# Performance work log

Measured on AMD Instinct MI355X. Metric: run time of the kernel, lower is better.

Reference implementation:

```python
import jax, jax.numpy as jnp
import numpy as np

IN_FEATURES = 4096
OUT_FEATURES = 4096
MAX_RANK = 32
ALPHA = 32
SCALING = ALPHA / MAX_RANK  # 1.0


def setup_inputs() -> dict:
    key = jax.random.key(0)
    k_x, k_u, k_v = jax.random.split(key, 3)
    x = jax.random.normal(k_x, (4, 2048, IN_FEATURES), dtype=jnp.float32)
    U = jax.random.normal(k_u, (OUT_FEATURES, MAX_RANK), dtype=jnp.float32) * 0.01
    S = jnp.ones((MAX_RANK,), dtype=jnp.float32)
    V = jax.random.normal(k_v, (MAX_RANK, IN_FEATURES), dtype=jnp.float32) * 0.01
    return {"x": x, "U": U, "S": S, "V": V}


def reference(x, U, S, V):
    # Original: W = U @ diag(S) @ V ; out = (x @ W.T) * scaling  (dropout=0 -> Identity)
    # Mathematically identical factored form: ((x @ V^T) * S) @ U^T * scaling.
    h = jnp.einsum('bsi,ri->bsr', x, V)        # [B,S,rank]
    h = h * S                                   # scale by singular values
    out = jnp.einsum('bsr,or->bso', h, U)       # [B,S,out]
    return out * SCALING
```

## Files before the change

kernel.cpp:

```cpp
#include <hip/hip_runtime.h>
#include <hip/hip_bf16.h>

typedef __bf16 bf16x8 __attribute__((ext_vector_type(8)));
typedef float  f32x4  __attribute__((ext_vector_type(4)));

#define IN_F   4096
#define OUT_F  4096
#define RANK   32

__device__ __forceinline__ bf16x8 cvt8(float4 a, float4 b) {
    bf16x8 r;
    r[0] = (__bf16)a.x; r[1] = (__bf16)a.y; r[2] = (__bf16)a.z; r[3] = (__bf16)a.w;
    r[4] = (__bf16)b.x; r[5] = (__bf16)b.y; r[6] = (__bf16)b.z; r[7] = (__bf16)b.w;
    return r;
}

__device__ __forceinline__ void gl_lds16(const float* g, void* l) {
    __builtin_amdgcn_global_load_lds(
        (const __attribute__((address_space(1))) char*)g,
        (__attribute__((address_space(3))) char*)l, 16, 0, 0);
}

template <int KS>
__global__ __launch_bounds__(256, 2)
void lora_h(const float* __restrict__ X, const float* __restrict__ S,
            const float* __restrict__ V, float* __restrict__ Hpart)
{
    constexpr int F    = IN_F / KS;
    constexpr int NCHK = F / 64;

    __shared__ float4 XB[3][4][2][2][64];
    __shared__ float4 VB[3][2][2][2][64];

    const int tid  = threadIdx.x;
    const int wave = tid >> 6;
    const int lane = tid & 63;
    const int r    = lane & 15;
    const int kg   = lane >> 4;

    const int t0    = blockIdx.x * 64;
    const int fbase = blockIdx.y * F;

    const float s_lo = S[r];
    const float s_hi = S[16 + r];

    auto stage = [&](int c, int nb) {
        const int fc = fbase + ((c + blockIdx.x) & (NCHK - 1)) * 64;
        #pragma unroll
        for (int t = 0; t < 6; ++t) {
            const int inst = wave * 6 + t;
            if (inst < 16) {
                const int tt = inst >> 2, s = (inst >> 1) & 1, h2 = inst & 1;
                gl_lds16(X + (size_t)(t0 + tt * 16 + r) * IN_F
                           + fc + s * 32 + h2 * 16 + kg * 4,
                         (void*)&XB[nb][tt][s][h2][0]);
            } else {
                const int v = inst - 16;
                const int vr = v >> 2, s = (v >> 1) & 1, h2 = v & 1;
                gl_lds16(V + (size_t)(vr * 16 + r) * IN_F
                           + fc + s * 32 + h2 * 16 + kg * 4,
                         (void*)&VB[nb][vr][s][h2][0]);
            }
        }
    };

    const int h  = kg >> 1;
    const int qb = (kg & 1) * 2;

    f32x4 acc[2] = {};

    auto compute = [&](int cur) {
        #pragma unroll
        for (int s = 0; s < 2; ++s) {
            float4 x0 = *(const float4*)&XB[cur][wave][s][h][qb * 16 + r];
            float4 x1 = *(const float4*)&XB[cur][wave][s][h][(qb + 1) * 16 + r];
            bf16x8 xb = cvt8(x0, x1);
            #pragma unroll
            for (int rh = 0; rh < 2; ++rh) {
                float4 v0 = *(const float4*)&VB[cur][rh][s][h][qb * 16 + r];
                float4 v1 = *(const float4*)&VB[cur][rh][s][h][(qb + 1) * 16 + r];
                acc[rh] = __builtin_amdgcn_mfma_f32_16x16x32_bf16(
                              xb, cvt8(v0, v1), acc[rh], 0, 0, 0);
            }
        }
    };

    stage(0, 0);
    stage(1, 1);

    for (int c = 0; c < NCHK; ++c) {
        if (c + 2 < NCHK) {
            stage(c + 2, (c + 2) % 3);
            asm volatile("s_waitcnt vmcnt(12)" ::: "memory");
        } else if (c + 1 < NCHK) {
            asm volatile("s_waitcnt vmcnt(6)" ::: "memory");
        } else {
            asm volatile("s_waitcnt vmcnt(0)" ::: "memory");
        }
        __builtin_amdgcn_s_barrier();
        __builtin_amdgcn_sched_barrier(0);
        compute(c % 3);
        __builtin_amdgcn_s_barrier();
    }

    float* Hq = Hpart + ((size_t)blockIdx.y * 8192 + t0) * RANK;
    #pragma unroll
    for (int j = 0; j < 4; ++j) {
        const int tok = wave * 16 + kg * 4 + j;
        Hq[(size_t)tok * RANK + r]      = acc[0][j] * s_lo;
        Hq[(size_t)tok * RANK + 16 + r] = acc[1][j] * s_hi;
    }
}

template <int NKS>
__global__ __launch_bounds__(256)
void lora_hred(const float* __restrict__ Hpart, float* __restrict__ H)
{
    const int idx = blockIdx.x * 256 + threadIdx.x;
    const float4* hp = reinterpret_cast<const float4*>(Hpart);
    float4 v = hp[idx];
    #pragma unroll
    for (int k = 1; k < NKS; ++k) {
        float4 p = hp[(size_t)k * 65536 + idx];
        v.x += p.x; v.y += p.y; v.z += p.z; v.w += p.w;
    }
    reinterpret_cast<float4*>(H)[idx] = v;
}

__global__ __launch_bounds__(256, 4)
void lora_out(const float* __restrict__ H, const float* __restrict__ U,
              float* __restrict__ Out)
{
    __shared__ float Hs[128][33];

    const int tid  = threadIdx.x;
    const int wave = tid >> 6;
    const int lane = tid & 63;
    const int r    = lane & 15;
    const int kg   = lane >> 4;

    const int tt = blockIdx.x >> 6;
    const int cq = blockIdx.x & 63;
    const int t0 = tt * 128;
    const int c0 = cq * 64;

    float4 ua[4][2];
    #pragma unroll
    for (int b = 0; b < 4; ++b) {
        const float4* up = reinterpret_cast<const float4*>(
            U + (size_t)(c0 + b * 16 + r) * RANK + kg * 8);
        ua[b][0] = up[0];
        ua[b][1] = up[1];
    }

    const float4* hsrc = reinterpret_cast<const float4*>(H + (size_t)t0 * RANK);
    #pragma unroll
    for (int k4 = 0; k4 < 4; ++k4) {
        const int fidx = tid + k4 * 256;
        float4 v = hsrc[fidx];
        const int tok = fidx >> 3;
        const int rr  = (fidx & 7) * 4;
        Hs[tok][rr] = v.x; Hs[tok][rr + 1] = v.y;
        Hs[tok][rr + 2] = v.z; Hs[tok][rr + 3] = v.w;
    }
    __syncthreads();

    bf16x8 ub[4];
    #pragma unroll
    for (int b = 0; b < 4; ++b) ub[b] = cvt8(ua[b][0], ua[b][1]);

    #pragma unroll
    for (int ai = 0; ai < 2; ++ai) {
        const int a = wave + ai * 4;
        bf16x8 hb;
        #pragma unroll
        for (int j = 0; j < 8; ++j) hb[j] = (__bf16)Hs[a * 16 + r][kg * 8 + j];
        float* orow = Out + (size_t)(t0 + a * 16 + r) * OUT_F + c0 + kg * 4;
        #pragma unroll
        for (int b = 0; b < 4; ++b) {
            f32x4 d = {0.f, 0.f, 0.f, 0.f};
            d = __builtin_amdgcn_mfma_f32_16x16x32_bf16(ub[b], hb, d, 0, 0, 0);
            *reinterpret_cast<float4*>(orow + b * 16) = *reinterpret_cast<float4*>(&d);
        }
    }
}

extern "C" void kernel_launch(void* const* d_in, const int* in_sizes, int n_in,
                              void* d_out, int out_size, void* d_ws, size_t ws_size,
                              hipStream_t stream) {
    const float* X = (const float*)d_in[0];
    const float* U = (const float*)d_in[1];
    const float* S = (const float*)d_in[2];
    const float* V = (const float*)d_in[3];
    float* Out = (float*)d_out;

    float* H     = (float*)d_ws;
    float* Hpart = (float*)d_ws + 262144;

    if (ws_size >= (size_t)5 * 1024 * 1024) {
        lora_h<4><<<dim3(128, 4), 256, 0, stream>>>(X, S, V, Hpart);
        lora_hred<4><<<256, 256, 0, stream>>>(Hpart, H);
        lora_out<<<4096, 256, 0, stream>>>(H, U, Out);
    } else {
        lora_h<1><<<dim3(128, 1), 256, 0, stream>>>(X, S, V, H);
        lora_out<<<4096, 256, 0, stream>>>(H, U, Out);
    }
}
```

Measured before the change: 68.32 us.

## Retile LoRA kernels: V in registers, 32-token blocks, wider output tiles

```diff
diff --git a/kernel.cpp b/kernel.cpp
--- a/kernel.cpp
+++ b/kernel.cpp
@@ -27,10 +27,9 @@
             const float* __restrict__ V, float* __restrict__ Hpart)
 {
     constexpr int F    = IN_F / KS;
-    constexpr int NCHK = F / 64;
-
-    __shared__ float4 XB[3][4][2][2][64];
-    __shared__ float4 VB[3][2][2][2][64];
+    constexpr int NCHK = F / 256;
+
+    __shared__ float4 XB[2][2][8][2][64];
 
     const int tid  = threadIdx.x;
     const int wave = tid >> 6;
@@ -38,78 +37,71 @@
     const int r    = lane & 15;
     const int kg   = lane >> 4;
 
-    const int t0    = blockIdx.x * 64;
+    const int tt = wave & 1;
+    const int rh = wave >> 1;
+
+    const int t0    = blockIdx.x * 32;
     const int fbase = blockIdx.y * F;
 
-    const float s_lo = S[r];
-    const float s_hi = S[16 + r];
-
     auto stage = [&](int c, int nb) {
-        const int fc = fbase + ((c + blockIdx.x) & (NCHK - 1)) * 64;
-        #pragma unroll
-        for (int t = 0; t < 6; ++t) {
-            const int inst = wave * 6 + t;
-            if (inst < 16) {
-                const int tt = inst >> 2, s = (inst >> 1) & 1, h2 = inst & 1;
-                gl_lds16(X + (size_t)(t0 + tt * 16 + r) * IN_F
-                           + fc + s * 32 + h2 * 16 + kg * 4,
-                         (void*)&XB[nb][tt][s][h2][0]);
-            } else {
-                const int v = inst - 16;
-                const int vr = v >> 2, s = (v >> 1) & 1, h2 = v & 1;
-                gl_lds16(V + (size_t)(vr * 16 + r) * IN_F
-                           + fc + s * 32 + h2 * 16 + kg * 4,
-                         (void*)&VB[nb][vr][s][h2][0]);
-            }
+        const int fc = fbase + ((c + blockIdx.x) & (NCHK - 1)) * 256;
+        #pragma unroll
+        for (int t = 0; t < 8; ++t) {
+            const int inst = wave * 8 + t;
+            const int ti = inst >> 4, s = (inst >> 1) & 7, h2 = inst & 1;
+            gl_lds16(X + (size_t)(t0 + ti * 16 + r) * IN_F
+                       + fc + s * 32 + h2 * 16 + kg * 4,
+                     (void*)&XB[nb][ti][s][h2][0]);
+        }
+    };
+
+    float4 vv[16];
+    auto vload = [&](int c) {
+        const int fc = fbase + ((c + blockIdx.x) & (NCHK - 1)) * 256;
+        const float* vrow = V + (size_t)(rh * 16 + r) * IN_F + fc + kg * 8;
+        #pragma unroll
+        for (int s = 0; s < 8; ++s) {
+            const float4* vp = reinterpret_cast<const float4*>(vrow + s * 32);
+            vv[2 * s]     = vp[0];
+            vv[2 * s + 1] = vp[1];
         }
     };
 
     const int h  = kg >> 1;
     const int qb = (kg & 1) * 2;
 
-    f32x4 acc[2] = {};
+    f32x4 acc = {0.f, 0.f, 0.f, 0.f};
 
     auto compute = [&](int cur) {
         #pragma unroll
-        for (int s = 0; s < 2; ++s) {
-            float4 x0 = *(const float4*)&XB[cur][wave][s][h][qb * 16 + r];
-            float4 x1 = *(const float4*)&XB[cur][wave][s][h][(qb + 1) * 16 + r];
-            bf16x8 xb = cvt8(x0, x1);
-            #pragma unroll
-            for (int rh = 0; rh < 2; ++rh) {
-                float4 v0 = *(const float4*)&VB[cur][rh][s][h][qb * 16 + r];
-                float4 v1 = *(const float4*)&VB[cur][rh][s][h][(qb + 1) * 16 + r];
-                acc[rh] = __builtin_amdgcn_mfma_f32_16x16x32_bf16(
-                              xb, cvt8(v0, v1), acc[rh], 0, 0, 0);
-            }
+        for (int s = 0; s < 8; ++s) {
+            float4 x0 = *(const float4*)&XB[cur][tt][s][h][qb * 16 + r];
+            float4 x1 = *(const float4*)&XB[cur][tt][s][h][(qb + 1) * 16 + r];
+            acc = __builtin_amdgcn_mfma_f32_16x16x32_bf16(
+                      cvt8(x0, x1), cvt8(vv[2 * s], vv[2 * s + 1]), acc, 0, 0, 0);
         }
     };
 
     stage(0, 0);
-    stage(1, 1);
-
     for (int c = 0; c < NCHK; ++c) {
-        if (c + 2 < NCHK) {
-            stage(c + 2, (c + 2) % 3);
-            asm volatile("s_waitcnt vmcnt(12)" ::: "memory");
-        } else if (c + 1 < NCHK) {
-            asm volatile("s_waitcnt vmcnt(6)" ::: "memory");
+        vload(c);
+        if (c + 1 < NCHK) {
+            stage(c + 1, (c + 1) & 1);
+            asm volatile("s_waitcnt vmcnt(8)" ::: "memory");
         } else {
             asm volatile("s_waitcnt vmcnt(0)" ::: "memory");
         }
         __builtin_amdgcn_s_barrier();
         __builtin_amdgcn_sched_barrier(0);
-        compute(c % 3);
+        compute(c & 1);
         __builtin_amdgcn_s_barrier();
     }
 
-    float* Hq = Hpart + ((size_t)blockIdx.y * 8192 + t0) * RANK;
-    #pragma unroll
-    for (int j = 0; j < 4; ++j) {
-        const int tok = wave * 16 + kg * 4 + j;
-        Hq[(size_t)tok * RANK + r]      = acc[0][j] * s_lo;
-        Hq[(size_t)tok * RANK + 16 + r] = acc[1][j] * s_hi;
-    }
+    const float sr = S[rh * 16 + r];
+    float* Hq = Hpart + ((size_t)blockIdx.y * 8192 + t0 + tt * 16) * RANK;
+    #pragma unroll
+    for (int j = 0; j < 4; ++j)
+        Hq[(size_t)(kg * 4 + j) * RANK + rh * 16 + r] = acc[j] * sr;
 }
 
 template <int NKS>
@@ -131,7 +123,7 @@
 void lora_out(const float* __restrict__ H, const float* __restrict__ U,
               float* __restrict__ Out)
 {
-    __shared__ float Hs[128][33];
+    __shared__ float Hs[32][33];
 
     const int tid  = threadIdx.x;
     const int wave = tid >> 6;
@@ -139,48 +131,49 @@
     const int r    = lane & 15;
     const int kg   = lane >> 4;
 
-    const int tt = blockIdx.x >> 6;
-    const int cq = blockIdx.x & 63;
-    const int t0 = tt * 128;
-    const int c0 = cq * 64;
-
-    float4 ua[4][2];
-    #pragma unroll
-    for (int b = 0; b < 4; ++b) {
-        const float4* up = reinterpret_cast<const float4*>(
-            U + (size_t)(c0 + b * 16 + r) * RANK + kg * 8);
-        ua[b][0] = up[0];
-        ua[b][1] = up[1];
-    }
-
-    const float4* hsrc = reinterpret_cast<const float4*>(H + (size_t)t0 * RANK);
-    #pragma unroll
-    for (int k4 = 0; k4 < 4; ++k4) {
-        const int fidx = tid + k4 * 256;
-        float4 v = hsrc[fidx];
-        const int tok = fidx >> 3;
-        const int rr  = (fidx & 7) * 4;
+    const int tt = blockIdx.x >> 2;
+    const int cq = blockIdx.x & 3;
+    const int t0 = tt * 32;
+
+    {
+        float4 v = reinterpret_cast<const float4*>(H + (size_t)t0 * RANK)[tid];
+        const int tok = tid >> 3;
+        const int rr  = (tid & 7) * 4;
         Hs[tok][rr] = v.x; Hs[tok][rr + 1] = v.y;
         Hs[tok][rr + 2] = v.z; Hs[tok][rr + 3] = v.w;
     }
     __syncthreads();
 
-    bf16x8 ub[4];
-    #pragma unroll
-    for (int b = 0; b < 4; ++b) ub[b] = cvt8(ua[b][0], ua[b][1]);
-
-    #pragma unroll
-    for (int ai = 0; ai < 2; ++ai) {
-        const int a = wave + ai * 4;
-        bf16x8 hb;
-        #pragma unroll
-        for (int j = 0; j < 8; ++j) hb[j] = (__bf16)Hs[a * 16 + r][kg * 8 + j];
-        float* orow = Out + (size_t)(t0 + a * 16 + r) * OUT_F + c0 + kg * 4;
+    bf16x8 hb[2];
+    #pragma unroll
+    for (int a = 0; a < 2; ++a)
+        #pragma unroll
+        for (int j = 0; j < 8; ++j) hb[a][j] = (__bf16)Hs[a * 16 + r][kg * 8 + j];
+
+    const int wc0 = cq * 1024 + wave * 256;
+
+    #pragma unroll
+    for (int g = 0; g < 4; ++g) {
+        float4 u0[4], u1[4];
         #pragma unroll
         for (int b = 0; b < 4; ++b) {
-            f32x4 d = {0.f, 0.f, 0.f, 0.f};
-            d = __builtin_amdgcn_mfma_f32_16x16x32_bf16(ub[b], hb, d, 0, 0, 0);
-            *reinterpret_cast<float4*>(orow + b * 16) = *reinterpret_cast<float4*>(&d);
+            const float4* up = reinterpret_cast<const float4*>(
+                U + (size_t)(wc0 + g * 64 + b * 16 + r) * RANK + kg * 8);
+            u0[b] = up[0];
+            u1[b] = up[1];
+        }
+        #pragma unroll
+        for (int b = 0; b < 4; ++b) {
+            bf16x8 ub = cvt8(u0[b], u1[b]);
+            #pragma unroll
+            for (int a = 0; a < 2; ++a) {
+                f32x4 d = {0.f, 0.f, 0.f, 0.f};
+                d = __builtin_amdgcn_mfma_f32_16x16x32_bf16(ub, hb[a], d, 0, 0, 0);
+                *reinterpret_cast<float4*>(
+                    Out + (size_t)(t0 + a * 16 + r) * OUT_F
+                        + wc0 + g * 64 + b * 16 + kg * 4)
+                    = *reinterpret_cast<float4*>(&d);
+            }
         }
     }
 }
@@ -197,12 +190,12 @@
     float* H     = (float*)d_ws;
     float* Hpart = (float*)d_ws + 262144;
 
-    if (ws_size >= (size_t)5 * 1024 * 1024) {
-        lora_h<4><<<dim3(128, 4), 256, 0, stream>>>(X, S, V, Hpart);
-        lora_hred<4><<<256, 256, 0, stream>>>(Hpart, H);
-        lora_out<<<4096, 256, 0, stream>>>(H, U, Out);
+    if (ws_size >= (size_t)3 * 1024 * 1024) {
+        lora_h<2><<<dim3(256, 2), 256, 0, stream>>>(X, S, V, Hpart);
+        lora_hred<2><<<256, 256, 0, stream>>>(Hpart, H);
+        lora_out<<<1024, 256, 0, stream>>>(H, U, Out);
     } else {
-        lora_h<1><<<dim3(128, 1), 256, 0, stream>>>(X, S, V, H);
-        lora_out<<<4096, 256, 0, stream>>>(H, U, Out);
-    }
-}
+        lora_h<1><<<dim3(256, 1), 256, 0, stream>>>(X, S, V, H);
+        lora_out<<<1024, 256, 0, stream>>>(H, U, Out);
+    }
+}
```

Result: slower. 90.97 us (+33.2%).

## Retile output kernel to 32 tokens by 1024 columns per block

Applied to the files above, without the earlier changes.

```diff
diff --git a/kernel.cpp b/kernel.cpp
--- a/kernel.cpp
+++ b/kernel.cpp
@@ -131,7 +131,7 @@
 void lora_out(const float* __restrict__ H, const float* __restrict__ U,
               float* __restrict__ Out)
 {
-    __shared__ float Hs[128][33];
+    __shared__ float Hs[32][33];
 
     const int tid  = threadIdx.x;
     const int wave = tid >> 6;
@@ -139,48 +139,49 @@
     const int r    = lane & 15;
     const int kg   = lane >> 4;
 
-    const int tt = blockIdx.x >> 6;
-    const int cq = blockIdx.x & 63;
-    const int t0 = tt * 128;
-    const int c0 = cq * 64;
-
-    float4 ua[4][2];
-    #pragma unroll
-    for (int b = 0; b < 4; ++b) {
-        const float4* up = reinterpret_cast<const float4*>(
-            U + (size_t)(c0 + b * 16 + r) * RANK + kg * 8);
-        ua[b][0] = up[0];
-        ua[b][1] = up[1];
-    }
-
-    const float4* hsrc = reinterpret_cast<const float4*>(H + (size_t)t0 * RANK);
-    #pragma unroll
-    for (int k4 = 0; k4 < 4; ++k4) {
-        const int fidx = tid + k4 * 256;
-        float4 v = hsrc[fidx];
-        const int tok = fidx >> 3;
-        const int rr  = (fidx & 7) * 4;
+    const int tt = blockIdx.x >> 2;
+    const int cq = blockIdx.x & 3;
+    const int t0 = tt * 32;
+
+    {
+        float4 v = reinterpret_cast<const float4*>(H + (size_t)t0 * RANK)[tid];
+        const int tok = tid >> 3;
+        const int rr  = (tid & 7) * 4;
         Hs[tok][rr] = v.x; Hs[tok][rr + 1] = v.y;
         Hs[tok][rr + 2] = v.z; Hs[tok][rr + 3] = v.w;
     }
     __syncthreads();
 
-    bf16x8 ub[4];
-    #pragma unroll
-    for (int b = 0; b < 4; ++b) ub[b] = cvt8(ua[b][0], ua[b][1]);
-
-    #pragma unroll
-    for (int ai = 0; ai < 2; ++ai) {
-        const int a = wave + ai * 4;
-        bf16x8 hb;
-        #pragma unroll
-        for (int j = 0; j < 8; ++j) hb[j] = (__bf16)Hs[a * 16 + r][kg * 8 + j];
-        float* orow = Out + (size_t)(t0 + a * 16 + r) * OUT_F + c0 + kg * 4;
+    bf16x8 hb[2];
+    #pragma unroll
+    for (int a = 0; a < 2; ++a)
+        #pragma unroll
+        for (int j = 0; j < 8; ++j) hb[a][j] = (__bf16)Hs[a * 16 + r][kg * 8 + j];
+
+    const int wc0 = cq * 1024 + wave * 256;
+
+    #pragma unroll
+    for (int g = 0; g < 4; ++g) {
+        float4 u0[4], u1[4];
         #pragma unroll
         for (int b = 0; b < 4; ++b) {
-            f32x4 d = {0.f, 0.f, 0.f, 0.f};
-            d = __builtin_amdgcn_mfma_f32_16x16x32_bf16(ub[b], hb, d, 0, 0, 0);
-            *reinterpret_cast<float4*>(orow + b * 16) = *reinterpret_cast<float4*>(&d);
+            const float4* up = reinterpret_cast<const float4*>(
+                U + (size_t)(wc0 + g * 64 + b * 16 + r) * RANK + kg * 8);
+            u0[b] = up[0];
+            u1[b] = up[1];
+        }
+        #pragma unroll
+        for (int b = 0; b < 4; ++b) {
+            bf16x8 ub = cvt8(u0[b], u1[b]);
+            #pragma unroll
+            for (int a = 0; a < 2; ++a) {
+                f32x4 d = {0.f, 0.f, 0.f, 0.f};
+                d = __builtin_amdgcn_mfma_f32_16x16x32_bf16(ub, hb[a], d, 0, 0, 0);
+                *reinterpret_cast<float4*>(
+                    Out + (size_t)(t0 + a * 16 + r) * OUT_F
+                        + wc0 + g * 64 + b * 16 + kg * 4)
+                    = *reinterpret_cast<float4*>(&d);
+            }
         }
     }
 }
@@ -200,9 +201,9 @@
     if (ws_size >= (size_t)5 * 1024 * 1024) {
         lora_h<4><<<dim3(128, 4), 256, 0, stream>>>(X, S, V, Hpart);
         lora_hred<4><<<256, 256, 0, stream>>>(Hpart, H);
-        lora_out<<<4096, 256, 0, stream>>>(H, U, Out);
+        lora_out<<<1024, 256, 0, stream>>>(H, U, Out);
     } else {
         lora_h<1><<<dim3(128, 1), 256, 0, stream>>>(X, S, V, H);
-        lora_out<<<4096, 256, 0, stream>>>(H, U, Out);
-    }
-}
+        lora_out<<<1024, 256, 0, stream>>>(H, U, Out);
+    }
+}
```

After: 66.97 us. 1.02x faster.
